# Optimization experiments

Hardware: AMD Instinct MI355X
Metric: run time of the kernel (lower is better)

The kernel has to match this reference:

```python
import jax, jax.numpy as jnp
import numpy as np

O, T, DIN, H, DOUT = 50000, 100000, 128, 512, 128


def _kaiming(k, fan_in, fan_out):
    return jax.random.normal(k, (fan_in, fan_out), jnp.float32) * np.sqrt(2.0 / fan_in)


def _bias(k, n, fan_in):
    b = 1.0 / np.sqrt(fan_in)
    return jax.random.uniform(k, (n,), jnp.float32, -b, b)


def setup_inputs() -> dict:
    key = jax.random.key(0)
    ks = jax.random.split(key, 16)
    return {
        "obj_vecs": jax.random.normal(ks[0], (O, DIN), jnp.float32),
        "pred_vecs": jax.random.normal(ks[1], (T, DIN), jnp.float32),
        "edges": jax.random.randint(ks[2], (T, 2), 0, O, jnp.int64 if jax.config.jax_enable_x64 else jnp.int32),
        # net1: Linear(3*DIN -> H), ReLU, Linear(H -> 2H+DOUT), ReLU
        "n1_w1": _kaiming(ks[3], 3 * DIN, H), "n1_b1": _bias(ks[4], H, 3 * DIN),
        "n1_w2": _kaiming(ks[5], H, 2 * H + DOUT), "n1_b2": _bias(ks[6], 2 * H + DOUT, H),
        # net2: Linear(H -> H), ReLU, Linear(H -> DOUT), ReLU
        "n2_w1": _kaiming(ks[7], H, H), "n2_b1": _bias(ks[8], H, H),
        "n2_w2": _kaiming(ks[9], H, DOUT), "n2_b2": _bias(ks[10], DOUT, H),
        # initial_obj_projection_layer: Linear(DIN -> H)
        "proj_w": _kaiming(ks[11], DIN, H), "proj_b": _bias(ks[12], H, DIN),
        # W_sim: Linear(H -> H)
        "sim_w": _kaiming(ks[13], H, H), "sim_b": _bias(ks[14], H, H),
    }


def reference(obj_vecs, pred_vecs, edges,
              n1_w1, n1_b1, n1_w2, n1_b2,
              n2_w1, n2_b1, n2_w2, n2_b2,
              proj_w, proj_b, sim_w, sim_b):
    n_obj = obj_vecs.shape[0]
    s_idx, o_idx = edges[:, 0], edges[:, 1]

    # net1 over concatenated triples  (T, 3*DIN) -> (T, 2H+DOUT)
    t_in = jnp.concatenate([obj_vecs[s_idx], pred_vecs, obj_vecs[o_idx]], axis=1)
    new_t = jax.nn.relu(jax.nn.relu(t_in @ n1_w1 + n1_b1) @ n1_w2 + n1_b2)
    new_s = new_t[:, :H]                 # (T, H) subject messages
    new_p = new_t[:, H:H + DOUT]         # (T, DOUT) new predicate vecs
    new_o = new_t[:, H + DOUT:]          # (T, H) object messages

    # attention query per node: W_sim(initial_obj_projection(obj_vecs))
    prev = obj_vecs @ proj_w + proj_b          # (O, H)
    prev_proj = prev @ sim_w + sim_b           # (O, H)

    # candidate messages for each node = subject-role msgs + object-role msgs
    cand_idx = jnp.concatenate([s_idx, o_idx])           # (2T,)
    cand = jnp.concatenate([new_s, new_o], axis=0)       # (2T, H)
    cand_proj = cand @ sim_w + sim_b                     # (2T, H)
    scores = jnp.sum(cand_proj * prev_proj[cand_idx], axis=1)  # (2T,)

    # the prepended all-zero row per node: W_sim(0) = sim_b, score = sim_b . prev_proj[i]
    zero_scores = prev_proj @ sim_b                      # (O,)

    # segment softmax over {zero row} U {incident messages}; zero row adds only
    # to the denominator since its value vector is 0.
    seg_max = jax.ops.segment_max(scores, cand_idx, num_segments=n_obj)
    m = jnp.maximum(zero_scores, seg_max)                # (O,)
    w = jnp.exp(scores - m[cand_idx])                    # (2T,)
    denom = jnp.exp(zero_scores - m) + jax.ops.segment_sum(w, cand_idx, num_segments=n_obj)
    pooled = jax.ops.segment_sum(w[:, None] * cand, cand_idx, num_segments=n_obj) / denom[:, None]

    new_obj = jax.nn.relu(jax.nn.relu(pooled @ n2_w1 + n2_b1) @ n2_w2 + n2_b2)
    return new_obj, new_p
```

## Files before the change

### kernel.cpp

```cpp
#include <hip/hip_runtime.h>

typedef unsigned short u16;
typedef unsigned int u32;
typedef u16 u16x8 __attribute__((ext_vector_type(8)));
typedef __bf16 bf16x8 __attribute__((ext_vector_type(8)));
typedef float f32x4 __attribute__((ext_vector_type(4)));

#define O_N 50000
#define T_N 100000
#define HID 512
#define K1 384
#define BM 128
#define BN 128
#define BK 32
#define LDT 40

#define OF_F32 1
#define OF_HI 2
#define OF_LO 4

__device__ __forceinline__ u16 f2bf(float f) {
  u32 u = __float_as_uint(f);
  u += 0x7fffu + ((u >> 16) & 1u);
  return (u16)(u >> 16);
}
__device__ __forceinline__ float bf2f(u16 b) {
  return __uint_as_float(((u32)b) << 16);
}
__device__ __forceinline__ f32x4 mfma16(u16x8 a, u16x8 b, f32x4 c) {
  return __builtin_amdgcn_mfma_f32_16x16x32_bf16(
      __builtin_bit_cast(bf16x8, a), __builtin_bit_cast(bf16x8, b), c, 0, 0, 0);
}
__device__ __forceinline__ float wave_sum(float v) {
#pragma unroll
  for (int m = 32; m >= 1; m >>= 1) v += __shfl_xor(v, m, 64);
  return v;
}

template <int AMODE, int BSPLIT, int RELU, int OFLAGS, int FUSE>
__global__ __launch_bounds__(256) void gemm_k(
    const void* __restrict__ Ap, const u16* __restrict__ Apl,
    const u16* __restrict__ Bph, const u16* __restrict__ Bpl,
    const float* __restrict__ biasf,
    float* __restrict__ Cf, u16* __restrict__ Ch, u16* __restrict__ Cl,
    u16* __restrict__ Ch2, u16* __restrict__ Cl2,
    int M, int N, int K, int lda, int ldc,
    const int* __restrict__ edges, const float* __restrict__ objf,
    const float* __restrict__ predf, int r0) {
  const bool ASPLIT = (AMODE == 1 || AMODE == 2 || AMODE == 3);
  __shared__ u16 Ah[BM * LDT];
  __shared__ u16 Al[(AMODE == 1 || AMODE == 2 || AMODE == 3) ? BM * LDT : 8];
  __shared__ u16 Bh[BN * LDT];
  __shared__ u16 Bl[BSPLIT ? BN * LDT : 8];

  const int tid = threadIdx.x;
  const int lane = tid & 63;
  const int wave = tid >> 6;
  const int wm = (wave >> 1) * 64;
  const int wn = (wave & 1) * 64;
  const int m0 = blockIdx.x * BM;
  const int n0 = blockIdx.y * BN;
  const int sr = tid >> 1;
  const int sh = (tid & 1) * 16;

  f32x4 acc[4][4] = {};

  for (int k0 = 0; k0 < K; k0 += BK) {
    __syncthreads();
    if (AMODE == 0) {
      u16x8 v0 = {0, 0, 0, 0, 0, 0, 0, 0}, v1 = {0, 0, 0, 0, 0, 0, 0, 0};
      if (m0 + sr < M) {
        const u16* src = (const u16*)Ap + (size_t)(m0 + sr) * lda + k0 + sh;
        v0 = *(const u16x8*)src;
        v1 = *(const u16x8*)(src + 8);
      }
      *(u16x8*)&Ah[sr * LDT + sh] = v0;
      *(u16x8*)&Ah[sr * LDT + sh + 8] = v1;
    } else if (AMODE == 3) {
      u16x8 h0 = {0, 0, 0, 0, 0, 0, 0, 0}, h1 = h0, l0 = h0, l1 = h0;
      if (m0 + sr < M) {
        size_t base = (size_t)(m0 + sr) * lda + k0 + sh;
        h0 = *(const u16x8*)((const u16*)Ap + base);
        h1 = *(const u16x8*)((const u16*)Ap + base + 8);
        l0 = *(const u16x8*)(Apl + base);
        l1 = *(const u16x8*)(Apl + base + 8);
      }
      *(u16x8*)&Ah[sr * LDT + sh] = h0;
      *(u16x8*)&Ah[sr * LDT + sh + 8] = h1;
      *(u16x8*)&Al[sr * LDT + sh] = l0;
      *(u16x8*)&Al[sr * LDT + sh + 8] = l1;
    } else {
      float vals[16];
      if (m0 + sr < M) {
        const float* src;
        if (AMODE == 1) {
          src = (const float*)Ap + (size_t)(m0 + sr) * lda + k0 + sh;
        } else {
          int gr = r0 + m0 + sr;
          int col = k0 + sh;
          if (col < 128) src = objf + (size_t)edges[gr * 2] * 128 + col;
          else if (col < 256) src = predf + (size_t)gr * 128 + (col - 128);
          else src = objf + (size_t)edges[gr * 2 + 1] * 128 + (col - 256);
        }
        const f32x4* s4 = (const f32x4*)src;
        f32x4 a0 = s4[0], a1 = s4[1], a2 = s4[2], a3 = s4[3];
#pragma unroll
        for (int i = 0; i < 4; i++) {
          vals[i] = a0[i]; vals[4 + i] = a1[i]; vals[8 + i] = a2[i]; vals[12 + i] = a3[i];
        }
      } else {
#pragma unroll
        for (int i = 0; i < 16; i++) vals[i] = 0.f;
      }
      u16x8 h0, h1, l0, l1;
#pragma unroll
      for (int i = 0; i < 8; i++) {
        u16 hb = f2bf(vals[i]);
        h0[i] = hb; l0[i] = f2bf(vals[i] - bf2f(hb));
        u16 hb2 = f2bf(vals[8 + i]);
        h1[i] = hb2; l1[i] = f2bf(vals[8 + i] - bf2f(hb2));
      }
      *(u16x8*)&Ah[sr * LDT + sh] = h0;
      *(u16x8*)&Ah[sr * LDT + sh + 8] = h1;
      *(u16x8*)&Al[sr * LDT + sh] = l0;
      *(u16x8*)&Al[sr * LDT + sh + 8] = l1;
    }
    {
      size_t base = (size_t)(n0 + sr) * K + k0 + sh;
      u16x8 b0 = *(const u16x8*)(Bph + base);
      u16x8 b1 = *(const u16x8*)(Bph + base + 8);
      *(u16x8*)&Bh[sr * LDT + sh] = b0;
      *(u16x8*)&Bh[sr * LDT + sh + 8] = b1;
      if (BSPLIT) {
        u16x8 c0 = *(const u16x8*)(Bpl + base);
        u16x8 c1 = *(const u16x8*)(Bpl + base + 8);
        *(u16x8*)&Bl[sr * LDT + sh] = c0;
        *(u16x8*)&Bl[sr * LDT + sh + 8] = c1;
      }
    }
    __syncthreads();
    const int fr = lane & 15;
    const int q8 = (lane >> 4) * 8;
    u16x8 af[4], bf[4];
#pragma unroll
    for (int i = 0; i < 4; i++) af[i] = *(const u16x8*)&Ah[(wm + i * 16 + fr) * LDT + q8];
#pragma unroll
    for (int j = 0; j < 4; j++) bf[j] = *(const u16x8*)&Bh[(wn + j * 16 + fr) * LDT + q8];
#pragma unroll
    for (int i = 0; i < 4; i++)
#pragma unroll
      for (int j = 0; j < 4; j++) acc[i][j] = mfma16(af[i], bf[j], acc[i][j]);
    if (ASPLIT) {
      u16x8 alf[4];
#pragma unroll
      for (int i = 0; i < 4; i++) alf[i] = *(const u16x8*)&Al[(wm + i * 16 + fr) * LDT + q8];
#pragma unroll
      for (int i = 0; i < 4; i++)
#pragma unroll
        for (int j = 0; j < 4; j++) acc[i][j] = mfma16(alf[i], bf[j], acc[i][j]);
    }
    if (BSPLIT) {
      u16x8 blf[4];
#pragma unroll
      for (int j = 0; j < 4; j++) blf[j] = *(const u16x8*)&Bl[(wn + j * 16 + fr) * LDT + q8];
#pragma unroll
      for (int i = 0; i < 4; i++)
#pragma unroll
        for (int j = 0; j < 4; j++) acc[i][j] = mfma16(af[i], blf[j], acc[i][j]);
    }
  }
  const int fc = lane & 15;
  const int fr4 = (lane >> 4) * 4;
#pragma unroll
  for (int j = 0; j < 4; j++) {
    int col = n0 + wn + j * 16 + fc;
    float bv = biasf ? biasf[col] : 0.f;
#pragma unroll
    for (int i = 0; i < 4; i++) {
      int rbase = m0 + wm + i * 16 + fr4;
#pragma unroll
      for (int rr = 0; rr < 4; rr++) {
        int row = rbase + rr;
        if (row < M) {
          float v = acc[i][j][rr] + bv;
          if (RELU) v = fmaxf(v, 0.f);
          if (FUSE) {
            if (col < 512) {
              size_t ci = (size_t)row * 512 + col;
              u16 h = f2bf(v);
              Ch[ci] = h;
              Cl[ci] = f2bf(v - bf2f(h));
            } else if (col < 640) {
              Cf[(size_t)row * 128 + (col - 512)] = v;
            } else {
              size_t ci = (size_t)row * 512 + (col - 640);
              u16 h = f2bf(v);
              Ch2[ci] = h;
              Cl2[ci] = f2bf(v - bf2f(h));
            }
          } else {
            size_t ci = (size_t)row * ldc + col;
            if (OFLAGS & OF_F32) Cf[ci] = v;
            if (OFLAGS & OF_HI) {
              u16 h = f2bf(v);
              Ch[ci] = h;
              if (OFLAGS & OF_LO) Cl[ci] = f2bf(v - bf2f(h));
            }
          }
        }
      }
    }
  }
}

__global__ void k_convT(const float* __restrict__ in, u16* __restrict__ outh,
                        u16* __restrict__ outl, int K, int N) {
  int idx = blockIdx.x * 256 + threadIdx.x;
  if (idx >= K * N) return;
  int n = idx / K, k = idx % K;
  float v = in[(size_t)k * N + n];
  u16 h = f2bf(v);
  outh[idx] = h;
  if (outl) outl[idx] = f2bf(v - bf2f(h));
}

__global__ void k_conv(const float* __restrict__ in, u16* __restrict__ outh,
                       u16* __restrict__ outl, int n) {
  int idx = blockIdx.x * 256 + threadIdx.x;
  if (idx >= n) return;
  float v = in[idx];
  u16 h = f2bf(v);
  outh[idx] = h;
  if (outl) outl[idx] = f2bf(v - bf2f(h));
}

__global__ void k_foldb1(const float* __restrict__ bp, const float* __restrict__ Ws,
                         const float* __restrict__ bs, float* __restrict__ bf1) {
  int n = blockIdx.x * 256 + threadIdx.x;
  if (n >= HID) return;
  float s = bs[n];
  for (int k = 0; k < HID; k++) s += bp[k] * Ws[(size_t)k * HID + n];
  bf1[n] = s;
}
__global__ void k_foldba(const float* __restrict__ bf1, const float* __restrict__ Ws,
                         float* __restrict__ ba) {
  int n = blockIdx.x * 256 + threadIdx.x;
  if (n >= HID) return;
  float s = 0.f;
  for (int k = 0; k < HID; k++) s += bf1[k] * Ws[(size_t)n * HID + k];
  ba[n] = s;
}
__global__ void k_foldwz(const float* __restrict__ Wf, const float* __restrict__ bs,
                         const float* __restrict__ bf1, float* __restrict__ wz,
                         float* __restrict__ bz) {
  int m = blockIdx.x * 256 + threadIdx.x;
  if (m < 128) {
    float s = 0.f;
    for (int n = 0; n < HID; n++) s += Wf[(size_t)m * HID + n] * bs[n];
    wz[m] = s;
  }
  if (m == 128) {
    float s = 0.f;
    for (int n = 0; n < HID; n++) s += bf1[n] * bs[n];
    *bz = s;
  }
}
__global__ void k_zsm(const float* __restrict__ obj, const float* __restrict__ wz,
                      const float* __restrict__ bz, float* __restrict__ zs, int rows) {
  int o = blockIdx.x * 4 + (threadIdx.x >> 6);
  int lane = threadIdx.x & 63;
  if (o >= rows) return;
  const float2* row = (const float2*)(obj + (size_t)o * 128);
  float2 v = row[lane];
  float2 w = ((const float2*)wz)[lane];
  float d = v.x * w.x + v.y * w.y;
  d = wave_sum(d);
  if (lane == 0) zs[o] = d + *bz;
}

__global__ void k_count(const int* __restrict__ edges, int* __restrict__ cnt) {
  int e = blockIdx.x * 256 + threadIdx.x;
  if (e >= 2 * T_N) return;
  int c = (e < T_N) ? edges[e * 2 + 0] : edges[(e - T_N) * 2 + 1];
  atomicAdd(cnt + c, 1);
}

__global__ void k_scan_a(const int* __restrict__ cnt, int* __restrict__ incl,
                         int* __restrict__ bsum) {
  __shared__ int sb[1024];
  int i = blockIdx.x * 1024 + threadIdx.x;
  int v = (i < O_N) ? cnt[i] : 0;
  sb[threadIdx.x] = v;
  __syncthreads();
  for (int ofs = 1; ofs < 1024; ofs <<= 1) {
    int t = (threadIdx.x >= ofs) ? sb[threadIdx.x - ofs] : 0;
    __syncthreads();
    sb[threadIdx.x] += t;
    __syncthreads();
  }
  if (i < O_N) incl[i] = sb[threadIdx.x];
  if (threadIdx.x == 1023) bsum[blockIdx.x] = sb[1023];
}

__global__ void k_scan_b(const int* __restrict__ bsum, int* __restrict__ bpre, int nb) {
  if (threadIdx.x == 0 && blockIdx.x == 0) {
    int run = 0;
    for (int b = 0; b < nb; b++) { bpre[b] = run; run += bsum[b]; }
  }
}

__global__ void k_scan_c(const int* __restrict__ incl, const int* __restrict__ cnt,
                         const int* __restrict__ bpre, int* __restrict__ excl,
                         int* __restrict__ cursor) {
  int i = blockIdx.x * 1024 + threadIdx.x;
  if (i >= O_N) return;
  int ex = incl[i] - cnt[i] + bpre[blockIdx.x];
  excl[i] = ex;
  cursor[i] = ex;
}

__global__ void k_fill(const int* __restrict__ edges, int* __restrict__ cursor,
                       int* __restrict__ csr) {
  int e = blockIdx.x * 256 + threadIdx.x;
  if (e >= 2 * T_N) return;
  int c = (e < T_N) ? edges[e * 2 + 0] : edges[(e - T_N) * 2 + 1];
  int pos = atomicAdd(cursor + c, 1);
  csr[pos] = e;
}

__global__ void k_scores(const u16* __restrict__ newShi, const u16* __restrict__ newOhi,
                         const u16* __restrict__ Slo, const u16* __restrict__ Olo,
                         const u16* __restrict__ auxhi, const float* __restrict__ zs,
                         const int* __restrict__ edges, float* __restrict__ scores,
                         int r0, int rows) {
  int idx = blockIdx.x * 4 + (threadIdx.x >> 6);
  int lane = threadIdx.x & 63;
  int rl = idx >> 1, side = idx & 1;
  if (rl >= rows) return;
  int grow = r0 + rl;
  int c = edges[grow * 2 + side];
  u16x8 ch = *(const u16x8*)((side ? newOhi : newShi) + (size_t)grow * HID + lane * 8);
  u16x8 cl = *(const u16x8*)((side ? Olo : Slo) + (size_t)rl * HID + lane * 8);
  u16x8 ah = *(const u16x8*)(auxhi + (size_t)c * HID + lane * 8);
  float d = 0.f;
#pragma unroll
  for (int k = 0; k < 8; k++) d += (bf2f(ch[k]) + bf2f(cl[k])) * bf2f(ah[k]);
  d = wave_sum(d);
  if (lane == 0) scores[(side ? T_N : 0) + grow] = d + zs[c];
}

__global__ void k_fix(const u16* __restrict__ newShi, const u16* __restrict__ newOhi,
                      const u16* __restrict__ auxhi, const float* __restrict__ auxf,
                      const int* __restrict__ csr, const int* __restrict__ excl,
                      const int* __restrict__ cnt, float* __restrict__ scores,
                      int q0, int rows) {
  int ol = blockIdx.x * 4 + (threadIdx.x >> 6);
  int lane = threadIdx.x & 63;
  if (ol >= rows) return;
  int o = q0 + ol;
  int off = excl[o], deg = cnt[o];
  if (deg == 0) return;
  const f32x4* afp = (const f32x4*)(auxf + (size_t)ol * HID + lane * 8);
  f32x4 af0 = afp[0], af1 = afp[1];
  u16x8 ah = *(const u16x8*)(auxhi + (size_t)o * HID + lane * 8);
  float al[8];
#pragma unroll
  for (int k = 0; k < 4; k++) {
    al[k] = af0[k] - bf2f(ah[k]);
    al[4 + k] = af1[k] - bf2f(ah[4 + k]);
  }
  for (int i = 0; i < deg; i++) {
    int e = csr[off + i];
    const u16* cand =
        (e < T_N) ? newShi + (size_t)e * HID : newOhi + (size_t)(e - T_N) * HID;
    u16x8 ch = *(const u16x8*)(cand + lane * 8);
    float d = 0.f;
#pragma unroll
    for (int k = 0; k < 8; k++) d += bf2f(ch[k]) * al[k];
    d = wave_sum(d);
    if (lane == 0) scores[e] += d;
  }
}

__global__ void k_pool(const u16* __restrict__ newShi, const u16* __restrict__ newOhi,
                       const float* __restrict__ scores, const float* __restrict__ zs,
                       const int* __restrict__ csr, const int* __restrict__ excl,
                       const int* __restrict__ cnt, float* __restrict__ pooledf,
                       int q0, int rows) {
  int ol = blockIdx.x * 4 + (threadIdx.x >> 6);
  int lane = threadIdx.x & 63;
  if (ol >= rows) return;
  int o = q0 + ol;
  int off = excl[o], deg = cnt[o];
  float zso = zs[o];
  float m = zso;
  for (int base = 0; base < deg; base += 64) {
    float s = (base + lane < deg) ? scores[csr[off + base + lane]] : -3.4e38f;
    m = fmaxf(m, s);
  }
#pragma unroll
  for (int x = 32; x >= 1; x >>= 1) m = fmaxf(m, __shfl_xor(m, x, 64));
  float denom = __expf(zso - m);
  float acc[8] = {0, 0, 0, 0, 0, 0, 0, 0};
  for (int i = 0; i < deg; i++) {
    int e = csr[off + i];
    float w = __expf(scores[e] - m);
    denom += w;
    const u16* cand =
        (e < T_N) ? newShi + (size_t)e * HID : newOhi + (size_t)(e - T_N) * HID;
    u16x8 cv = *(const u16x8*)(cand + lane * 8);
#pragma unroll
    for (int k = 0; k < 8; k++) acc[k] += w * bf2f(cv[k]);
  }
  float inv = 1.0f / denom;
  f32x4 o0, o1;
#pragma unroll
  for (int k = 0; k < 4; k++) {
    o0[k] = acc[k] * inv;
    o1[k] = acc[4 + k] * inv;
  }
  f32x4* dst = (f32x4*)(pooledf + (size_t)ol * HID + lane * 8);
  dst[0] = o0;
  dst[1] = o1;
}

extern "C" void kernel_launch(void* const* d_in, const int* in_sizes, int n_in,
                              void* d_out, int out_size, void* d_ws, size_t ws_size,
                              hipStream_t stream) {
  const float* objf = (const float*)d_in[0];
  const float* predf = (const float*)d_in[1];
  const int* edges = (const int*)d_in[2];
  const float* n1w1f = (const float*)d_in[3];
  const float* n1b1f = (const float*)d_in[4];
  const float* n1w2f = (const float*)d_in[5];
  const float* n1b2f = (const float*)d_in[6];
  const float* n2w1f = (const float*)d_in[7];
  const float* n2b1f = (const float*)d_in[8];
  const float* n2w2f = (const float*)d_in[9];
  const float* n2b2f = (const float*)d_in[10];
  const float* projwf = (const float*)d_in[11];
  const float* projbf = (const float*)d_in[12];
  const float* simwf = (const float*)d_in[13];
  const float* simbf = (const float*)d_in[14];

  float* out_obj = (float*)d_out;
  float* out_p = (float*)d_out + (size_t)O_N * 128;

  const long long FIXED = 267000000ll;
  long long budget = (long long)ws_size - FIXED;
  if (budget < 5000000ll) budget = 5000000ll;
  long long rT_l = budget / 4096;  if (rT_l > 26000) rT_l = 26000;
  int rT = (int)(rT_l & ~127ll);   if (rT < 1280) rT = 1280;
  long long rOb_l = budget / 3072; if (rOb_l > 25000) rOb_l = 25000;
  int rOb = (int)rOb_l;            if (rOb < 1280) rOb = 1280;
  long long rFx_l = budget / 2048; if (rFx_l > 25000) rFx_l = 25000;
  int rFx = (int)rFx_l;            if (rFx < 1280) rFx = 1280;
  const int nT = (T_N + rT - 1) / rT;
  const int nOb = (O_N + rOb - 1) / rOb;
  const int nFx = (O_N + rFx - 1) / rFx;
  size_t arena_sz = (size_t)rT * 4096;
  if ((size_t)rOb * 3072 > arena_sz) arena_sz = (size_t)rOb * 3072;
  if ((size_t)rFx * 2048 > arena_sz) arena_sz = (size_t)rFx * 2048;
  arena_sz = (arena_sz + 4095) & ~(size_t)4095;

  char* ws = (char*)d_ws;
  size_t off = 0;
  u16* newShi = (u16*)(ws + off); off += (size_t)T_N * HID * 2;
  u16* newOhi = (u16*)(ws + off); off += (size_t)T_N * HID * 2;
  u16* auxhi = (u16*)(ws + off);  off += (size_t)O_N * HID * 2;
  char* arena = ws + off; off += arena_sz;

  u16* h1H = (u16*)arena;
  u16* h1L = (u16*)(arena + (size_t)rT * HID * 2);
  u16* Slo = (u16*)(arena + (size_t)rT * HID * 4);
  u16* Olo = (u16*)(arena + (size_t)rT * HID * 6);
  float* auxfC = (float*)arena;
  float* pooledf = (float*)arena;
  u16* h2c = (u16*)(arena + (size_t)rOb * HID * 4);

  float* scoresb = (float*)(ws + off); off += (size_t)2 * T_N * 4;
  float* zsb = (float*)(ws + off); off += (size_t)O_N * 4;
  int* cnt = (int*)(ws + off); off += (size_t)O_N * 4;
  int* incl = (int*)(ws + off); off += (size_t)O_N * 4;
  int* excl = (int*)(ws + off); off += (size_t)O_N * 4;
  int* cursor = (int*)(ws + off); off += (size_t)O_N * 4;
  int* csr = (int*)(ws + off); off += (size_t)2 * T_N * 4;
  int* bsum = (int*)(ws + off); off += 4096;
  int* bpre = (int*)(ws + off); off += 4096;
  u16* w1TH = (u16*)(ws + off); off += (size_t)K1 * HID * 2;
  u16* w1TL = (u16*)(ws + off); off += (size_t)K1 * HID * 2;
  u16* w2TH = (u16*)(ws + off); off += (size_t)1152 * HID * 2;
  u16* w2TL = (u16*)(ws + off); off += (size_t)1152 * HID * 2;
  u16* swTH = (u16*)(ws + off); off += (size_t)HID * HID * 2;
  u16* swTL = (u16*)(ws + off); off += (size_t)HID * HID * 2;
  u16* swRH = (u16*)(ws + off); off += (size_t)HID * HID * 2;
  u16* swRL = (u16*)(ws + off); off += (size_t)HID * HID * 2;
  u16* a2TH = (u16*)(ws + off); off += (size_t)HID * HID * 2;
  u16* a2TL = (u16*)(ws + off); off += (size_t)HID * HID * 2;
  u16* b2TH = (u16*)(ws + off); off += (size_t)128 * HID * 2;
  u16* b2TL = (u16*)(ws + off); off += (size_t)128 * HID * 2;
  float* Wf = (float*)(ws + off);  off += (size_t)128 * HID * 4;
  float* Waf = (float*)(ws + off); off += (size_t)128 * HID * 4;
  u16* WaTH = (u16*)(ws + off); off += (size_t)HID * 128 * 2;
  u16* WaTL = (u16*)(ws + off); off += (size_t)HID * 128 * 2;
  float* bf1 = (float*)(ws + off); off += 2048;
  float* baf = (float*)(ws + off); off += 2048;
  float* wzf = (float*)(ws + off); off += 512;
  float* bzf = (float*)(ws + off); off += 16;

  hipMemsetAsync(cnt, 0, O_N * sizeof(int), stream);

  k_convT<<<768, 256, 0, stream>>>(n1w1f, w1TH, w1TL, K1, HID);
  k_convT<<<2304, 256, 0, stream>>>(n1w2f, w2TH, w2TL, HID, 1152);
  k_convT<<<1024, 256, 0, stream>>>(simwf, swTH, swTL, HID, HID);
  k_conv<<<1024, 256, 0, stream>>>(simwf, swRH, swRL, HID * HID);
  k_convT<<<1024, 256, 0, stream>>>(n2w1f, a2TH, a2TL, HID, HID);
  k_convT<<<256, 256, 0, stream>>>(n2w2f, b2TH, b2TL, HID, 128);

  k_count<<<782, 256, 0, stream>>>(edges, cnt);
  k_scan_a<<<49, 1024, 0, stream>>>(cnt, incl, bsum);
  k_scan_b<<<1, 64, 0, stream>>>(bsum, bpre, 49);
  k_scan_c<<<49, 1024, 0, stream>>>(incl, cnt, bpre, excl, cursor);
  k_fill<<<782, 256, 0, stream>>>(edges, cursor, csr);

  {
    dim3 gW(1, 4);
    gemm_k<1, 1, 0, OF_F32, 0><<<gW, 256, 0, stream>>>(
        projwf, nullptr, swTH, swTL, nullptr,
        Wf, nullptr, nullptr, nullptr, nullptr,
        128, HID, HID, HID, HID, nullptr, nullptr, nullptr, 0);
    gemm_k<1, 1, 0, OF_F32, 0><<<gW, 256, 0, stream>>>(
        Wf, nullptr, swRH, swRL, nullptr,
        Waf, nullptr, nullptr, nullptr, nullptr,
        128, HID, HID, HID, HID, nullptr, nullptr, nullptr, 0);
    k_convT<<<256, 256, 0, stream>>>(Waf, WaTH, WaTL, 128, HID);
    k_foldb1<<<2, 256, 0, stream>>>(projbf, simwf, simbf, bf1);
    k_foldba<<<2, 256, 0, stream>>>(bf1, simwf, baf);
    k_foldwz<<<1, 256, 0, stream>>>(Wf, simbf, bf1, wzf, bzf);
  }

  {
    dim3 gA((O_N + BM - 1) / BM, 4);
    gemm_k<1, 1, 0, OF_HI, 0><<<gA, 256, 0, stream>>>(
        objf, nullptr, WaTH, WaTL, baf,
        nullptr, auxhi, nullptr, nullptr, nullptr,
        O_N, HID, 128, 128, HID, nullptr, nullptr, nullptr, 0);
    k_zsm<<<(O_N + 3) / 4, 256, 0, stream>>>(objf, wzf, bzf, zsb, O_N);
  }

  for (int ci = 0; ci < nT; ci++) {
    int r0 = ci * rT;
    int rows = (r0 + rT <= T_N) ? rT : (T_N - r0);
    dim3 g4((rows + BM - 1) / BM, 4);
    dim3 g9((rows + BM - 1) / BM, 9);
    gemm_k<2, 1, 1, OF_HI | OF_LO, 0><<<g4, 256, 0, stream>>>(
        nullptr, nullptr, w1TH, w1TL, n1b1f,
        nullptr, h1H, h1L, nullptr, nullptr,
        rows, HID, K1, 0, HID, edges, objf, predf, r0);
    gemm_k<3, 1, 1, 0, 1><<<g9, 256, 0, stream>>>(
        h1H, h1L, w2TH, w2TL, n1b2f,
        out_p + (size_t)r0 * 128, newShi + (size_t)r0 * HID, Slo,
        newOhi + (size_t)r0 * HID, Olo,
        rows, 1152, HID, HID, HID, nullptr, nullptr, nullptr, 0);
    k_scores<<<(2 * rows + 3) / 4, 256, 0, stream>>>(
        newShi, newOhi, Slo, Olo, auxhi, zsb, edges, scoresb, r0, rows);
  }

  for (int ci = 0; ci < nFx; ci++) {
    int q0 = ci * rFx;
    int rows = (q0 + rFx <= O_N) ? rFx : (O_N - q0);
    dim3 g4((rows + BM - 1) / BM, 4);
    gemm_k<1, 1, 0, OF_F32, 0><<<g4, 256, 0, stream>>>(
        objf + (size_t)q0 * 128, nullptr, WaTH, WaTL, baf,
        auxfC, nullptr, nullptr, nullptr, nullptr,
        rows, HID, 128, 128, HID, nullptr, nullptr, nullptr, 0);
    k_fix<<<(rows + 3) / 4, 256, 0, stream>>>(
        newShi, newOhi, auxhi, auxfC, csr, excl, cnt, scoresb, q0, rows);
  }

  for (int ci = 0; ci < nOb; ci++) {
    int q0 = ci * rOb;
    int rows = (q0 + rOb <= O_N) ? rOb : (O_N - q0);
    dim3 g4((rows + BM - 1) / BM, 4);
    dim3 g1((rows + BM - 1) / BM, 1);
    k_pool<<<(rows + 3) / 4, 256, 0, stream>>>(
        newShi, newOhi, scoresb, zsb, csr, excl, cnt, pooledf, q0, rows);
    gemm_k<1, 1, 1, OF_HI, 0><<<g4, 256, 0, stream>>>(
        pooledf, nullptr, a2TH, a2TL, n2b1f,
        nullptr, h2c, nullptr, nullptr, nullptr,
        rows, HID, HID, HID, HID, nullptr, nullptr, nullptr, 0);
    gemm_k<0, 1, 1, OF_F32, 0><<<g1, 256, 0, stream>>>(
        h2c, nullptr, b2TH, b2TL, n2b2f,
        out_obj + (size_t)q0 * 128, nullptr, nullptr, nullptr, nullptr,
        rows, 128, HID, HID, 128, nullptr, nullptr, nullptr, 0);
  }

  (void)in_sizes; (void)n_in; (void)out_size;
}
```

Before: 2.013 ms.

## Fuse score dot-products into net1 second GEMM epilogue and drop lo-part stores

```diff
diff --git a/kernel.cpp b/kernel.cpp
--- a/kernel.cpp
+++ b/kernel.cpp
@@ -43,10 +43,11 @@
     const u16* __restrict__ Bph, const u16* __restrict__ Bpl,
     const float* __restrict__ biasf,
     float* __restrict__ Cf, u16* __restrict__ Ch, u16* __restrict__ Cl,
-    u16* __restrict__ Ch2, u16* __restrict__ Cl2,
+    u16* __restrict__ Ch2,
     int M, int N, int K, int lda, int ldc,
     const int* __restrict__ edges, const float* __restrict__ objf,
-    const float* __restrict__ predf, int r0) {
+    const float* __restrict__ predf, int r0,
+    const u16* __restrict__ auxp, float* __restrict__ scoresp) {
   const bool ASPLIT = (AMODE == 1 || AMODE == 2 || AMODE == 3);
   __shared__ u16 Ah[BM * LDT];
   __shared__ u16 Al[(AMODE == 1 || AMODE == 2 || AMODE == 3) ? BM * LDT : 8];
@@ -171,6 +172,58 @@
   }
   const int fc = lane & 15;
   const int fr4 = (lane >> 4) * 4;
+  if (FUSE) {
+    const int side = (n0 >= 640) ? 1 : (n0 < 512 ? 0 : -1);
+    const int cb = n0 + wn + fc;
+    float bvs[4];
+#pragma unroll
+    for (int j = 0; j < 4; j++) bvs[j] = biasf[cb + j * 16];
+    __syncthreads();
+    float* scb = (float*)Ah;
+#pragma unroll
+    for (int i = 0; i < 4; i++) {
+#pragma unroll
+      for (int rr = 0; rr < 4; rr++) {
+        int rl = wm + i * 16 + fr4 + rr;
+        int row = m0 + rl;
+        float sc = 0.f;
+        if (row < M) {
+          const u16* arow = nullptr;
+          if (side == 0) arow = auxp + (size_t)edges[(size_t)(r0 + row) * 2] * 512;
+          else if (side == 1) arow = auxp + (size_t)edges[(size_t)(r0 + row) * 2 + 1] * 512;
+#pragma unroll
+          for (int j = 0; j < 4; j++) {
+            int col = cb + j * 16;
+            float v = acc[i][j][rr] + bvs[j];
+            v = fmaxf(v, 0.f);
+            if (side < 0) {
+              Cf[(size_t)row * 128 + (col - 512)] = v;
+            } else {
+              int cc = col - (side ? 640 : 0);
+              size_t ci = (size_t)row * 512 + cc;
+              if (side) Ch2[ci] = f2bf(v);
+              else Ch[ci] = f2bf(v);
+              sc += v * bf2f(arow[cc]);
+            }
+          }
+        }
+        if (side >= 0) {
+#pragma unroll
+          for (int mm = 1; mm <= 8; mm <<= 1) sc += __shfl_xor(sc, mm, 64);
+          if (fc == 0) scb[rl * 2 + (wn ? 1 : 0)] = sc;
+        }
+      }
+    }
+    __syncthreads();
+    if (side >= 0 && tid < 128) {
+      int row = m0 + tid;
+      if (row < M) {
+        float s = scb[tid * 2] + scb[tid * 2 + 1];
+        atomicAdd(&scoresp[(side ? T_N : 0) + (r0 + row)], s);
+      }
+    }
+    return;
+  }
 #pragma unroll
   for (int j = 0; j < 4; j++) {
     int col = n0 + wn + j * 16 + fc;
@@ -184,28 +237,12 @@
         if (row < M) {
           float v = acc[i][j][rr] + bv;
           if (RELU) v = fmaxf(v, 0.f);
-          if (FUSE) {
-            if (col < 512) {
-              size_t ci = (size_t)row * 512 + col;
-              u16 h = f2bf(v);
-              Ch[ci] = h;
-              Cl[ci] = f2bf(v - bf2f(h));
-            } else if (col < 640) {
-              Cf[(size_t)row * 128 + (col - 512)] = v;
-            } else {
-              size_t ci = (size_t)row * 512 + (col - 640);
-              u16 h = f2bf(v);
-              Ch2[ci] = h;
-              Cl2[ci] = f2bf(v - bf2f(h));
-            }
-          } else {
-            size_t ci = (size_t)row * ldc + col;
-            if (OFLAGS & OF_F32) Cf[ci] = v;
-            if (OFLAGS & OF_HI) {
-              u16 h = f2bf(v);
-              Ch[ci] = h;
-              if (OFLAGS & OF_LO) Cl[ci] = f2bf(v - bf2f(h));
-            }
+          size_t ci = (size_t)row * ldc + col;
+          if (OFLAGS & OF_F32) Cf[ci] = v;
+          if (OFLAGS & OF_HI) {
+            u16 h = f2bf(v);
+            Ch[ci] = h;
+            if (OFLAGS & OF_LO) Cl[ci] = f2bf(v - bf2f(h));
           }
         }
       }
@@ -328,25 +365,12 @@
   csr[pos] = e;
 }
 
-__global__ void k_scores(const u16* __restrict__ newShi, const u16* __restrict__ newOhi,
-                         const u16* __restrict__ Slo, const u16* __restrict__ Olo,
-                         const u16* __restrict__ auxhi, const float* __restrict__ zs,
-                         const int* __restrict__ edges, float* __restrict__ scores,
-                         int r0, int rows) {
-  int idx = blockIdx.x * 4 + (threadIdx.x >> 6);
-  int lane = threadIdx.x & 63;
-  int rl = idx >> 1, side = idx & 1;
-  if (rl >= rows) return;
-  int grow = r0 + rl;
-  int c = edges[grow * 2 + side];
-  u16x8 ch = *(const u16x8*)((side ? newOhi : newShi) + (size_t)grow * HID + lane * 8);
-  u16x8 cl = *(const u16x8*)((side ? Olo : Slo) + (size_t)rl * HID + lane * 8);
-  u16x8 ah = *(const u16x8*)(auxhi + (size_t)c * HID + lane * 8);
-  float d = 0.f;
-#pragma unroll
-  for (int k = 0; k < 8; k++) d += (bf2f(ch[k]) + bf2f(cl[k])) * bf2f(ah[k]);
-  d = wave_sum(d);
-  if (lane == 0) scores[(side ? T_N : 0) + grow] = d + zs[c];
+__global__ void k_sinit(const int* __restrict__ edges, const float* __restrict__ zs,
+                        float* __restrict__ scores) {
+  int e = blockIdx.x * 256 + threadIdx.x;
+  if (e >= 2 * T_N) return;
+  int c = (e < T_N) ? edges[e * 2 + 0] : edges[(e - T_N) * 2 + 1];
+  scores[e] = zs[c];
 }
 
 __global__ void k_fix(const u16* __restrict__ newShi, const u16* __restrict__ newOhi,
@@ -385,8 +409,8 @@
 __global__ void k_pool(const u16* __restrict__ newShi, const u16* __restrict__ newOhi,
                        const float* __restrict__ scores, const float* __restrict__ zs,
                        const int* __restrict__ csr, const int* __restrict__ excl,
-                       const int* __restrict__ cnt, float* __restrict__ pooledf,
-                       int q0, int rows) {
+                       const int* __restrict__ cnt, u16* __restrict__ pooledH,
+                       u16* __restrict__ pooledL, int q0, int rows) {
   int ol = blockIdx.x * 4 + (threadIdx.x >> 6);
   int lane = threadIdx.x & 63;
   if (ol >= rows) return;
@@ -413,15 +437,16 @@
     for (int k = 0; k < 8; k++) acc[k] += w * bf2f(cv[k]);
   }
   float inv = 1.0f / denom;
-  f32x4 o0, o1;
-#pragma unroll
-  for (int k = 0; k < 4; k++) {
-    o0[k] = acc[k] * inv;
-    o1[k] = acc[4 + k] * inv;
-  }
-  f32x4* dst = (f32x4*)(pooledf + (size_t)ol * HID + lane * 8);
-  dst[0] = o0;
-  dst[1] = o1;
+  u16x8 ph, pl;
+#pragma unroll
+  for (int k = 0; k < 8; k++) {
+    float v = acc[k] * inv;
+    u16 h = f2bf(v);
+    ph[k] = h;
+    pl[k] = f2bf(v - bf2f(h));
+  }
+  *(u16x8*)(pooledH + (size_t)ol * HID + lane * 8) = ph;
+  *(u16x8*)(pooledL + (size_t)ol * HID + lane * 8) = pl;
 }
 
 extern "C" void kernel_launch(void* const* d_in, const int* in_sizes, int n_in,
@@ -449,18 +474,28 @@
   const long long FIXED = 267000000ll;
   long long budget = (long long)ws_size - FIXED;
   if (budget < 5000000ll) budget = 5000000ll;
-  long long rT_l = budget / 4096;  if (rT_l > 26000) rT_l = 26000;
-  int rT = (int)(rT_l & ~127ll);   if (rT < 1280) rT = 1280;
-  long long rOb_l = budget / 3072; if (rOb_l > 25000) rOb_l = 25000;
-  int rOb = (int)rOb_l;            if (rOb < 1280) rOb = 1280;
-  long long rFx_l = budget / 2048; if (rFx_l > 25000) rFx_l = 25000;
-  int rFx = (int)rFx_l;            if (rFx < 1280) rFx = 1280;
+  int rT, rOb, rFx;
+  {
+    long long r = budget / 2048; if (r > 50048) r = 50048; if (r < 1280) r = 1280;
+    int n = (int)((T_N + r - 1) / r);
+    rT = ((T_N + n - 1) / n + 127) & ~127;
+  }
+  {
+    long long r = budget / 3072; if (r > 25024) r = 25024; if (r < 1280) r = 1280;
+    int n = (int)((O_N + r - 1) / r);
+    rOb = ((O_N + n - 1) / n + 127) & ~127;
+  }
+  {
+    long long r = budget / 2048; if (r > 25024) r = 25024; if (r < 1280) r = 1280;
+    int n = (int)((O_N + r - 1) / r);
+    rFx = ((O_N + n - 1) / n + 127) & ~127;
+  }
   const int nT = (T_N + rT - 1) / rT;
   const int nOb = (O_N + rOb - 1) / rOb;
   const int nFx = (O_N + rFx - 1) / rFx;
-  size_t arena_sz = (size_t)rT * 4096;
+  size_t arena_sz = (size_t)rT * 2048;
+  if ((size_t)rFx * 2048 > arena_sz) arena_sz = (size_t)rFx * 2048;
   if ((size_t)rOb * 3072 > arena_sz) arena_sz = (size_t)rOb * 3072;
-  if ((size_t)rFx * 2048 > arena_sz) arena_sz = (size_t)rFx * 2048;
   arena_sz = (arena_sz + 4095) & ~(size_t)4095;
 
   char* ws = (char*)d_ws;
@@ -471,12 +506,11 @@
   char* arena = ws + off; off += arena_sz;
 
   u16* h1H = (u16*)arena;
-  u16* h1L = (u16*)(arena + (size_t)rT * HID * 2);
-  u16* Slo = (u16*)(arena + (size_t)rT * HID * 4);
-  u16* Olo = (u16*)(arena + (size_t)rT * HID * 6);
+  u16* h1L = (u16*)(arena + (size_t)rT * 1024);
   float* auxfC = (float*)arena;
-  float* pooledf = (float*)arena;
-  u16* h2c = (u16*)(arena + (size_t)rOb * HID * 4);
+  u16* pooledH = (u16*)arena;
+  u16* pooledL = (u16*)(arena + (size_t)rOb * 1024);
+  u16* h2c = (u16*)(arena + (size_t)rOb * 2048);
 
   float* scoresb = (float*)(ws + off); off += (size_t)2 * T_N * 4;
   float* zsb = (float*)(ws + off); off += (size_t)O_N * 4;
@@ -527,12 +561,12 @@
     dim3 gW(1, 4);
     gemm_k<1, 1, 0, OF_F32, 0><<<gW, 256, 0, stream>>>(
         projwf, nullptr, swTH, swTL, nullptr,
-        Wf, nullptr, nullptr, nullptr, nullptr,
-        128, HID, HID, HID, HID, nullptr, nullptr, nullptr, 0);
+        Wf, nullptr, nullptr, nullptr,
+        128, HID, HID, HID, HID, nullptr, nullptr, nullptr, 0, nullptr, nullptr);
     gemm_k<1, 1, 0, OF_F32, 0><<<gW, 256, 0, stream>>>(
         Wf, nullptr, swRH, swRL, nullptr,
-        Waf, nullptr, nullptr, nullptr, nullptr,
-        128, HID, HID, HID, HID, nullptr, nullptr, nullptr, 0);
+        Waf, nullptr, nullptr, nullptr,
+        128, HID, HID, HID, HID, nullptr, nullptr, nullptr, 0, nullptr, nullptr);
     k_convT<<<256, 256, 0, stream>>>(Waf, WaTH, WaTL, 128, HID);
     k_foldb1<<<2, 256, 0, stream>>>(projbf, simwf, simbf, bf1);
     k_foldba<<<2, 256, 0, stream>>>(bf1, simwf, baf);
@@ -543,10 +577,12 @@
     dim3 gA((O_N + BM - 1) / BM, 4);
     gemm_k<1, 1, 0, OF_HI, 0><<<gA, 256, 0, stream>>>(
         objf, nullptr, WaTH, WaTL, baf,
-        nullptr, auxhi, nullptr, nullptr, nullptr,
-        O_N, HID, 128, 128, HID, nullptr, nullptr, nullptr, 0);
+        nullptr, auxhi, nullptr, nullptr,
+        O_N, HID, 128, 128, HID, nullptr, nullptr, nullptr, 0, nullptr, nullptr);
     k_zsm<<<(O_N + 3) / 4, 256, 0, stream>>>(objf, wzf, bzf, zsb, O_N);
   }
+
+  k_sinit<<<782, 256, 0, stream>>>(edges, zsb, scoresb);
 
   for (int ci = 0; ci < nT; ci++) {
     int r0 = ci * rT;
@@ -555,15 +591,13 @@
     dim3 g9((rows + BM - 1) / BM, 9);
     gemm_k<2, 1, 1, OF_HI | OF_LO, 0><<<g4, 256, 0, stream>>>(
         nullptr, nullptr, w1TH, w1TL, n1b1f,
-        nullptr, h1H, h1L, nullptr, nullptr,
-        rows, HID, K1, 0, HID, edges, objf, predf, r0);
+        nullptr, h1H, h1L, nullptr,
+        rows, HID, K1, 0, HID, edges, objf, predf, r0, nullptr, nullptr);
     gemm_k<3, 1, 1, 0, 1><<<g9, 256, 0, stream>>>(
         h1H, h1L, w2TH, w2TL, n1b2f,
-        out_p + (size_t)r0 * 128, newShi + (size_t)r0 * HID, Slo,
-        newOhi + (size_t)r0 * HID, Olo,
-        rows, 1152, HID, HID, HID, nullptr, nullptr, nullptr, 0);
-    k_scores<<<(2 * rows + 3) / 4, 256, 0, stream>>>(
-        newShi, newOhi, Slo, Olo, auxhi, zsb, edges, scoresb, r0, rows);
+        out_p + (size_t)r0 * 128, newShi + (size_t)r0 * HID, nullptr,
+        newOhi + (size_t)r0 * HID,
+        rows, 1152, HID, HID, HID, edges, nullptr, nullptr, r0, auxhi, scoresb);
   }
 
   for (int ci = 0; ci < nFx; ci++) {
@@ -572,8 +606,8 @@
     dim3 g4((rows + BM - 1) / BM, 4);
     gemm_k<1, 1, 0, OF_F32, 0><<<g4, 256, 0, stream>>>(
         objf + (size_t)q0 * 128, nullptr, WaTH, WaTL, baf,
-        auxfC, nullptr, nullptr, nullptr, nullptr,
-        rows, HID, 128, 128, HID, nullptr, nullptr, nullptr, 0);
+        auxfC, nullptr, nullptr, nullptr,
+        rows, HID, 128, 128, HID, nullptr, nullptr, nullptr, 0, nullptr, nullptr);
     k_fix<<<(rows + 3) / 4, 256, 0, stream>>>(
         newShi, newOhi, auxhi, auxfC, csr, excl, cnt, scoresb, q0, rows);
   }
@@ -584,15 +618,15 @@
     dim3 g4((rows + BM - 1) / BM, 4);
     dim3 g1((rows + BM - 1) / BM, 1);
     k_pool<<<(rows + 3) / 4, 256, 0, stream>>>(
-        newShi, newOhi, scoresb, zsb, csr, excl, cnt, pooledf, q0, rows);
-    gemm_k<1, 1, 1, OF_HI, 0><<<g4, 256, 0, stream>>>(
-        pooledf, nullptr, a2TH, a2TL, n2b1f,
-        nullptr, h2c, nullptr, nullptr, nullptr,
-        rows, HID, HID, HID, HID, nullptr, nullptr, nullptr, 0);
+        newShi, newOhi, scoresb, zsb, csr, excl, cnt, pooledH, pooledL, q0, rows);
+    gemm_k<3, 1, 1, OF_HI, 0><<<g4, 256, 0, stream>>>(
+        pooledH, pooledL, a2TH, a2TL, n2b1f,
+        nullptr, h2c, nullptr, nullptr,
+        rows, HID, HID, HID, HID, nullptr, nullptr, nullptr, 0, nullptr, nullptr);
     gemm_k<0, 1, 1, OF_F32, 0><<<g1, 256, 0, stream>>>(
         h2c, nullptr, b2TH, b2TL, n2b2f,
-        out_obj + (size_t)q0 * 128, nullptr, nullptr, nullptr, nullptr,
-        rows, 128, HID, HID, 128, nullptr, nullptr, nullptr, 0);
+        out_obj + (size_t)q0 * 128, nullptr, nullptr, nullptr,
+        rows, 128, HID, HID, 128, nullptr, nullptr, nullptr, 0, nullptr, nullptr);
   }
 
   (void)in_sizes; (void)n_in; (void)out_size;
```

Result: faster. 1.905 ms (-5.3%).
